# Optimization experiments

Measured on AMD Instinct MI355X. Metric: run time of the kernel, lower is better.

The kernel has to match this reference:

```python
import jax, jax.numpy as jnp
import numpy as np

COST_CLASS = 1.0
COST_COORD = 1.0
ALPHA = 0.25
GAMMA = 2.0
EPS = 1e-8
B, N = 4, 512


def setup_inputs() -> dict:
    key = jax.random.key(0)
    k1, k2, k3 = jax.random.split(key, 3)
    return {
        "pred_logits": jax.random.normal(k1, (B, N), dtype=jnp.float32),
        "pred_points": jax.random.uniform(k2, (B, N, 2), dtype=jnp.float32),
        "gt_points": jax.random.uniform(k3, (B, N, 2), dtype=jnp.float32),
        "gt_mask": jnp.ones((B, N), dtype=bool),
    }


def _cost_matrix(pred_logits, pred_points, gt_points):
    # focal-style classification cost, depends only on the prediction -> column-constant
    prob = jax.nn.sigmoid(pred_logits)                       # [B, N]
    neg = (1.0 - ALPHA) * prob ** GAMMA * (-jnp.log(1.0 - prob + EPS))
    pos = ALPHA * (1.0 - prob) ** GAMMA * (-jnp.log(prob + EPS))
    cost_class = (pos - neg)[:, :, None]                     # [B, N, 1]
    # L1 cdist between pred_points and gt_points
    cost_coord = jnp.sum(
        jnp.abs(pred_points[:, :, None, :] - gt_points[:, None, :, :]), axis=-1
    )                                                        # [B, N, N]
    return COST_CLASS * cost_class + COST_COORD * cost_coord


def _lsa(cost):
    # Jonker-Volgenant shortest augmenting path (e-maxx Hungarian), square, minimization.
    c = np.asarray(cost, dtype=np.float64)
    n = c.shape[0]
    INF = 1e18
    u = np.zeros(n + 1)
    v = np.zeros(n + 1)
    p = np.zeros(n + 1, dtype=np.int64)   # p[j] = row matched to column j (1-based)
    way = np.zeros(n + 1, dtype=np.int64)
    for i in range(1, n + 1):
        p[0] = i
        j0 = 0
        minv = np.full(n + 1, INF)
        used = np.zeros(n + 1, dtype=bool)
        while True:
            used[j0] = True
            i0 = p[j0]
            cur = c[i0 - 1] - u[i0] - v[1:]
            nu = ~used[1:]
            mv = minv[1:]
            wy = way[1:]
            upd = nu & (cur < mv)
            mv[upd] = cur[upd]
            wy[upd] = j0
            cand = np.where(nu, mv, INF)
            j1 = int(np.argmin(cand)) + 1
            delta = cand[j1 - 1]
            u[p[used]] += delta
            v[used] -= delta
            mv[nu] -= delta
            j0 = j1
            if p[j0] == 0:
                break
        while j0:
            j1 = int(way[j0])
            p[j0] = int(p[j1])
            j0 = j1
    col_of_row = np.empty(n, dtype=np.int64)
    col_of_row[p[1:] - 1] = np.arange(n)
    return np.arange(n), col_of_row


def reference(pred_logits, pred_points, gt_points, gt_mask):
    C = _cost_matrix(pred_logits, pred_points, gt_points)   # [B, N, N]
    mask = np.asarray(gt_mask)
    assert mask.all(), "reference assumes all gt slots valid (static shapes)"
    Cn = np.asarray(jax.device_get(C))
    pred_idx, gt_idx = [], []
    for b in range(Cn.shape[0]):
        r, c = _lsa(Cn[b])
        pred_idx.append(r)
        gt_idx.append(c)
    pred_idx = jnp.asarray(np.stack(pred_idx))
    gt_idx = jnp.asarray(np.stack(gt_idx))
    return pred_idx, gt_idx, C
```

## Files before the change

kernel.cpp:

```cpp
#include <hip/hip_runtime.h>
#include <math.h>

constexpr int B_ = 4;
constexpr int N_ = 512;

__device__ __forceinline__ float cephes_expf(float xin) {
#pragma clang fp contract(off)
    float x = fminf(xin, 88.3762626647950f);
    x = fmaxf(x, -88.3762626647949f);
    float fx = x * 1.44269504088896341f;
    fx = fx + 0.5f;
    fx = floorf(fx);
    float tmp = fx * 0.693359375f;
    float z0  = fx * -2.12194440e-4f;
    float r = x - tmp;
    r = r - z0;
    float zz = r * r;
    float y = 1.9875691500E-4f;
    y = y * r + 1.3981999507E-3f;
    y = y * r + 8.3334519073E-3f;
    y = y * r + 4.1665795894E-2f;
    y = y * r + 1.6666665459E-1f;
    y = y * r + 5.0000001201E-1f;
    y = y * zz + r;
    y = y + 1.0f;
    int n = (int)fx;
    float p2n = __uint_as_float((unsigned)(n + 0x7f) << 23);
    float res = y * p2n;
    return fmaxf(res, xin);
}

__device__ __forceinline__ float cephes_logf(float t) {
#pragma clang fp contract(off)
    float xx = fmaxf(t, 1.17549435e-38f);
    unsigned u = __float_as_uint(xx);
    int e_i = (int)(u >> 23) - 0x7f;
    float e = (float)e_i + 1.0f;
    float m = __uint_as_float((u & 0x807fffffu) | 0x3f000000u);
    int mask = (m < 0.707106781186547524f);
    float tmp1 = mask ? m : 0.0f;
    float x = m - 1.0f;
    e = e - (mask ? 1.0f : 0.0f);
    x = x + tmp1;
    float z = x * x;
    float y = 7.0376836292E-2f;
    y = y * x + -1.1514610310E-1f;
    y = y * x + 1.1676998740E-1f;
    y = y * x + -1.2420140846E-1f;
    y = y * x + 1.4249322787E-1f;
    y = y * x + -1.6668057665E-1f;
    y = y * x + 2.0000714765E-1f;
    y = y * x + -2.4999993993E-1f;
    y = y * x + 3.3333331174E-1f;
    y = y * x;
    y = y * z;
    y = e * -2.12194440e-4f + y;
    y = y - z * 0.5f;
    float res = x + y;
    res = res + e * 0.693359375f;
    return res;
}

__global__ __launch_bounds__(256) void class_cost_kernel(
    const float* __restrict__ logits, float* __restrict__ cc_out)
{
#pragma clang fp contract(off)
    int idx = blockIdx.x * 256 + threadIdx.x;
    if (idx >= B_ * N_) return;
    float x    = logits[idx];
    float e    = cephes_expf(-x);
    float prob = 1.0f / (1.0f + e);
    float om   = 1.0f - prob;
    float p2   = prob * prob;
    float o2   = om * om;
    float lneg = cephes_logf(om   + 1e-8f);
    float lpos = cephes_logf(prob + 1e-8f);
    float neg  = (0.75f * p2) * (-lneg);
    float pos  = (0.25f * o2) * (-lpos);
    cc_out[idx] = pos - neg;
}

__global__ __launch_bounds__(512) void cost_kernel(
    const float* __restrict__ cc,
    const float* __restrict__ pred_pts,
    const float* __restrict__ gt_pts,
    float* __restrict__ C)
{
    int blk = blockIdx.x;
    int b = blk >> 9;
    int i = blk & (N_ - 1);
    int j = threadIdx.x;

    const float2* pp2 = reinterpret_cast<const float2*>(pred_pts);
    const float2* gp2 = reinterpret_cast<const float2*>(gt_pts);
    float2 pp = pp2[b * N_ + i];
    float2 gp = gp2[b * N_ + j];
    float coord = fabsf(pp.x - gp.x) + fabsf(pp.y - gp.y);

    C[(size_t)b * N_ * N_ + (size_t)i * N_ + j] = cc[blk] + coord;
}

template<int CTRL>
__device__ __forceinline__ uint32_t dpp32(uint32_t x) {
    return (uint32_t)__builtin_amdgcn_update_dpp((int)x, (int)x, CTRL, 0xF, 0xF, false);
}
#define UMINSTEP(X, CTRL) { uint32_t o_ = dpp32<CTRL>(X); X = (o_ < X) ? o_ : X; }

__device__ __forceinline__ uint32_t wave_umin_lane63(uint32_t x) {
    UMINSTEP(x, 0x111) UMINSTEP(x, 0x112) UMINSTEP(x, 0x114)
    UMINSTEP(x, 0x118) UMINSTEP(x, 0x142) UMINSTEP(x, 0x143)
    return x;
}

__device__ __forceinline__ double readlane_f64(double d, int lane) {
    unsigned long long ll = (unsigned long long)__double_as_longlong(d);
    unsigned lo = (unsigned)__builtin_amdgcn_readlane((int)(unsigned)ll, lane);
    unsigned hi = (unsigned)__builtin_amdgcn_readlane((int)(unsigned)(ll >> 32), lane);
    return __longlong_as_double((long long)(((unsigned long long)hi << 32) | lo));
}

__global__ __launch_bounds__(64) void solve_kernel(
    const float* __restrict__ cc_in,
    const float* __restrict__ pred_pts,
    const float* __restrict__ gt_pts,
    float* __restrict__ pred_idx,
    float* __restrict__ gt_idx)
{
    const int b = blockIdx.x;
    const int t = threadIdx.x;

    const float2* pq = reinterpret_cast<const float2*>(pred_pts) + b * N_;
    const float2* gq = reinterpret_cast<const float2*>(gt_pts)   + b * N_;
    const float*  cq = cc_in + b * N_;
    const int base = t << 3;

    float2 r0 = pq[base + 0], r1 = pq[base + 1], r2 = pq[base + 2], r3 = pq[base + 3];
    float2 r4 = pq[base + 4], r5 = pq[base + 5], r6 = pq[base + 6], r7 = pq[base + 7];
    float2 g0 = gq[base + 0], g1 = gq[base + 1], g2 = gq[base + 2], g3 = gq[base + 3];
    float2 g4 = gq[base + 4], g5 = gq[base + 5], g6 = gq[base + 6], g7 = gq[base + 7];
    float  c0 = cq[base + 0], c1 = cq[base + 1], c2 = cq[base + 2], c3 = cq[base + 3];
    float  c4 = cq[base + 4], c5 = cq[base + 5], c6 = cq[base + 6], c7 = cq[base + 7];

    double u0=0.0,u1=0.0,u2=0.0,u3=0.0,u4=0.0,u5=0.0,u6=0.0,u7=0.0;
    double v0=0.0,v1=0.0,v2=0.0,v3=0.0,v4=0.0,v5=0.0,v6=0.0,v7=0.0;
    int    p0=-1,p1=-1,p2=-1,p3=-1,p4=-1,p5=-1,p6=-1,p7=-1;

    #pragma unroll
    for (int k = 0; k < 8; ++k)
        pred_idx[b * N_ + t + 64 * k] = (float)(t + 64 * k);

    #define SEL8F(sl, x0,x1,x2,x3,x4,x5,x6,x7, out) {                      \
        float a0_=((sl)&1)?(x1):(x0), a1_=((sl)&1)?(x3):(x2);              \
        float a2_=((sl)&1)?(x5):(x4), a3_=((sl)&1)?(x7):(x6);              \
        float b0_=((sl)&2)?a1_:a0_,   b1_=((sl)&2)?a3_:a2_;                \
        out = ((sl)&4)?b1_:b0_; }
    #define SEL8I(sl, x0,x1,x2,x3,x4,x5,x6,x7, out) {                      \
        int a0_=((sl)&1)?(x1):(x0), a1_=((sl)&1)?(x3):(x2);                \
        int a2_=((sl)&1)?(x5):(x4), a3_=((sl)&1)?(x7):(x6);                \
        int b0_=((sl)&2)?a1_:a0_,   b1_=((sl)&2)?a3_:a2_;                  \
        out = ((sl)&4)?b1_:b0_; }
    #define SEL8D(sl, x0,x1,x2,x3,x4,x5,x6,x7, out) {                      \
        double a0_=((sl)&1)?(x1):(x0), a1_=((sl)&1)?(x3):(x2);             \
        double a2_=((sl)&1)?(x5):(x4), a3_=((sl)&1)?(x7):(x6);             \
        double b0_=((sl)&2)?a1_:a0_,   b1_=((sl)&2)?a3_:a2_;               \
        out = ((sl)&4)?b1_:b0_; }

    float px_r, py_r, cc_r; double urow;
    #define ROW_SCALARS(r) {                                               \
        int sl_ = (r) & 7, ln_ = (r) >> 3;                                 \
        float sx_, sy_, sc_; double su_;                                   \
        SEL8F(sl_, r0.x,r1.x,r2.x,r3.x,r4.x,r5.x,r6.x,r7.x, sx_);          \
        SEL8F(sl_, r0.y,r1.y,r2.y,r3.y,r4.y,r5.y,r6.y,r7.y, sy_);          \
        SEL8F(sl_, c0,c1,c2,c3,c4,c5,c6,c7, sc_);                          \
        SEL8D(sl_, u0,u1,u2,u3,u4,u5,u6,u7, su_);                          \
        px_r = __uint_as_float((unsigned)__builtin_amdgcn_readlane(        \
                   (int)__float_as_uint(sx_), ln_));                       \
        py_r = __uint_as_float((unsigned)__builtin_amdgcn_readlane(        \
                   (int)__float_as_uint(sy_), ln_));                       \
        cc_r = __uint_as_float((unsigned)__builtin_amdgcn_readlane(        \
                   (int)__float_as_uint(sc_), ln_));                       \
        urow = readlane_f64(su_, ln_); }

    const float INF32 = __uint_as_float(0x7F800000u);

    for (int i = 0; i < N_; ++i) {
        unsigned used_m  = 0u;
        unsigned chain_m = (t == (i >> 3)) ? (1u << (i & 7)) : 0u;
        ROW_SCALARS(i);

        for (;;) {
#pragma clang fp contract(off)
            float w0 = cc_r + (fabsf(px_r - g0.x) + fabsf(py_r - g0.y));
            float w1 = cc_r + (fabsf(px_r - g1.x) + fabsf(py_r - g1.y));
            float w2 = cc_r + (fabsf(px_r - g2.x) + fabsf(py_r - g2.y));
            float w3 = cc_r + (fabsf(px_r - g3.x) + fabsf(py_r - g3.y));
            float w4 = cc_r + (fabsf(px_r - g4.x) + fabsf(py_r - g4.y));
            float w5 = cc_r + (fabsf(px_r - g5.x) + fabsf(py_r - g5.y));
            float w6 = cc_r + (fabsf(px_r - g6.x) + fabsf(py_r - g6.y));
            float w7 = cc_r + (fabsf(px_r - g7.x) + fabsf(py_r - g7.y));
            w0 = (used_m & 0x01u) ? INF32 : w0;
            w1 = (used_m & 0x02u) ? INF32 : w1;
            w2 = (used_m & 0x04u) ? INF32 : w2;
            w3 = (used_m & 0x08u) ? INF32 : w3;
            w4 = (used_m & 0x10u) ? INF32 : w4;
            w5 = (used_m & 0x20u) ? INF32 : w5;
            w6 = (used_m & 0x40u) ? INF32 : w6;
            w7 = (used_m & 0x80u) ? INF32 : w7;

            double d0 = ((double)w0 - urow) - v0;
            double d1 = ((double)w1 - urow) - v1;
            double d2 = ((double)w2 - urow) - v2;
            double d3 = ((double)w3 - urow) - v3;
            double d4 = ((double)w4 - urow) - v4;
            double d5 = ((double)w5 - urow) - v5;
            double d6 = ((double)w6 - urow) - v6;
            double d7 = ((double)w7 - urow) - v7;

            double  ka = (d1 < d0) ? d1 : d0;  uint32_t sa = (d1 < d0) ? 1u : 0u;
            double  kb = (d3 < d2) ? d3 : d2;  uint32_t sb = (d3 < d2) ? 3u : 2u;
            double  kx = (d5 < d4) ? d5 : d4;  uint32_t sx = (d5 < d4) ? 5u : 4u;
            double  kd = (d7 < d6) ? d7 : d6;  uint32_t sd = (d7 < d6) ? 7u : 6u;
            double  ke = (kb < ka) ? kb : ka;  uint32_t se = (kb < ka) ? sb : sa;
            double  kf = (kd < kx) ? kd : kx;  uint32_t sf = (kd < kx) ? sd : sx;
            double  bv = (kf < ke) ? kf : ke;  uint32_t bslot = (kf < ke) ? sf : se;

            uint64_t kb64 = (uint64_t)__double_as_longlong(bv);
            kb64 ^= (kb64 >> 63) ? 0xFFFFFFFFFFFFFFFFull : 0x8000000000000000ull;
            uint32_t khi = (uint32_t)(kb64 >> 32);
            uint32_t klo = (uint32_t)kb64;

            int own_pre;
            SEL8I(bslot, p0,p1,p2,p3,p4,p5,p6,p7, own_pre);

            uint32_t Mhi = (uint32_t)__builtin_amdgcn_readlane(
                               (int)wave_umin_lane63(khi), 63);
            unsigned long long tied_hi = __ballot(khi == Mhi);

            int lane1; uint32_t Mlo;
            if (__builtin_popcountll(tied_hi) == 1) {
                lane1 = (int)__builtin_ctzll(tied_hi);
                Mlo = (uint32_t)__builtin_amdgcn_readlane((int)klo, lane1);
            } else {
                uint32_t kl2 = (khi == Mhi) ? klo : 0xFFFFFFFFu;
                Mlo = (uint32_t)__builtin_amdgcn_readlane(
                          (int)wave_umin_lane63(kl2), 63);
                lane1 = (int)__builtin_ctzll(__ballot(khi == Mhi && klo == Mlo));
            }

            int slot1 = __builtin_amdgcn_readlane((int)bslot, lane1);
            int owner = __builtin_amdgcn_readlane(own_pre, lane1);

            uint64_t M = ((uint64_t)Mhi << 32) | Mlo;
            uint64_t db = (M >> 63) ? (M ^ 0x8000000000000000ull) : ~M;
            double delta = __longlong_as_double((long long)db);

            if (owner < 0) {
                u0 += (chain_m & 0x01u) ? delta : 0.0;
                u1 += (chain_m & 0x02u) ? delta : 0.0;
                u2 += (chain_m & 0x04u) ? delta : 0.0;
                u3 += (chain_m & 0x08u) ? delta : 0.0;
                u4 += (chain_m & 0x10u) ? delta : 0.0;
                u5 += (chain_m & 0x20u) ? delta : 0.0;
                u6 += (chain_m & 0x40u) ? delta : 0.0;
                u7 += (chain_m & 0x80u) ? delta : 0.0;
                v0 -= (used_m  & 0x01u) ? delta : 0.0;
                v1 -= (used_m  & 0x02u) ? delta : 0.0;
                v2 -= (used_m  & 0x04u) ? delta : 0.0;
                v3 -= (used_m  & 0x08u) ? delta : 0.0;
                v4 -= (used_m  & 0x10u) ? delta : 0.0;
                v5 -= (used_m  & 0x20u) ? delta : 0.0;
                v6 -= (used_m  & 0x40u) ? delta : 0.0;
                v7 -= (used_m  & 0x80u) ? delta : 0.0;
                bool mine = (t == lane1);
                p0 = (mine && slot1 == 0) ? i : p0;
                p1 = (mine && slot1 == 1) ? i : p1;
                p2 = (mine && slot1 == 2) ? i : p2;
                p3 = (mine && slot1 == 3) ? i : p3;
                p4 = (mine && slot1 == 4) ? i : p4;
                p5 = (mine && slot1 == 5) ? i : p5;
                p6 = (mine && slot1 == 6) ? i : p6;
                p7 = (mine && slot1 == 7) ? i : p7;
                break;
            }

            ROW_SCALARS(owner);

            u0 += (chain_m & 0x01u) ? delta : 0.0;
            u1 += (chain_m & 0x02u) ? delta : 0.0;
            u2 += (chain_m & 0x04u) ? delta : 0.0;
            u3 += (chain_m & 0x08u) ? delta : 0.0;
            u4 += (chain_m & 0x10u) ? delta : 0.0;
            u5 += (chain_m & 0x20u) ? delta : 0.0;
            u6 += (chain_m & 0x40u) ? delta : 0.0;
            u7 += (chain_m & 0x80u) ? delta : 0.0;
            v0 -= (used_m  & 0x01u) ? delta : 0.0;
            v1 -= (used_m  & 0x02u) ? delta : 0.0;
            v2 -= (used_m  & 0x04u) ? delta : 0.0;
            v3 -= (used_m  & 0x08u) ? delta : 0.0;
            v4 -= (used_m  & 0x10u) ? delta : 0.0;
            v5 -= (used_m  & 0x20u) ? delta : 0.0;
            v6 -= (used_m  & 0x40u) ? delta : 0.0;
            v7 -= (used_m  & 0x80u) ? delta : 0.0;

            used_m  |= (t == lane1)        ? (1u << slot1)       : 0u;
            chain_m |= (t == (owner >> 3)) ? (1u << (owner & 7)) : 0u;
        }
    }

    gt_idx[b * N_ + p0] = (float)(base);
    gt_idx[b * N_ + p1] = (float)(base + 1);
    gt_idx[b * N_ + p2] = (float)(base + 2);
    gt_idx[b * N_ + p3] = (float)(base + 3);
    gt_idx[b * N_ + p4] = (float)(base + 4);
    gt_idx[b * N_ + p5] = (float)(base + 5);
    gt_idx[b * N_ + p6] = (float)(base + 6);
    gt_idx[b * N_ + p7] = (float)(base + 7);
}

extern "C" void kernel_launch(void* const* d_in, const int* in_sizes, int n_in,
                              void* d_out, int out_size, void* d_ws, size_t ws_size,
                              hipStream_t stream)
{
    const float* logits   = (const float*)d_in[0];
    const float* pred_pts = (const float*)d_in[1];
    const float* gt_pts   = (const float*)d_in[2];

    float* out      = (float*)d_out;
    float* pred_idx = out;
    float* gt_idx   = out + B_ * N_;
    float* C        = out + 2 * B_ * N_;
    float* cc       = (float*)d_ws;

    class_cost_kernel<<<(B_ * N_ + 255) / 256, 256, 0, stream>>>(logits, cc);
    cost_kernel<<<B_ * N_, N_, 0, stream>>>(cc, pred_pts, gt_pts, C);
    solve_kernel<<<B_, 64, 0, stream>>>(cc, pred_pts, gt_pts, pred_idx, gt_idx);
}
```

Baseline: 1.645 ms.

## Run all batch solves in one block, co-locating waves on one SIMD

Launches the assignment solver as a single 1024-thread block and reads the hardware wave ID to find which SIMD each wave runs on. The four batch solves are assigned to waves that share the most populated SIMD; all other waves exit. This concentrates the serial solves on one CU/SIMD, possibly for shared cache locality, at the risk of the waves contending for one SIMD's issue bandwidth.

```diff
diff --git a/kernel.cpp b/kernel.cpp
--- a/kernel.cpp
+++ b/kernel.cpp
@@ -119,15 +119,46 @@
     return __longlong_as_double((long long)(((unsigned long long)hi << 32) | lo));
 }
 
-__global__ __launch_bounds__(64) void solve_kernel(
+#define HWID_GETREG_IMM (4 | (0 << 6) | (31 << 11))
+
+__global__ __launch_bounds__(1024) void solve_kernel(
     const float* __restrict__ cc_in,
     const float* __restrict__ pred_pts,
     const float* __restrict__ gt_pts,
     float* __restrict__ pred_idx,
     float* __restrict__ gt_idx)
 {
-    const int b = blockIdx.x;
-    const int t = threadIdx.x;
+    const int wave = threadIdx.x >> 6;
+    const int t    = threadIdx.x & 63;
+
+    unsigned hwid = (unsigned)__builtin_amdgcn_s_getreg(HWID_GETREG_IMM);
+    int my_simd = (int)((hwid >> 4) & 3u);
+
+    __shared__ int simd_of[16];
+    if (t == 0) simd_of[wave] = my_simd;
+    __syncthreads();
+
+    int cnt0 = 0, cnt1 = 0, cnt2 = 0, cnt3 = 0;
+    #pragma unroll
+    for (int w = 0; w < 16; ++w) {
+        int s = simd_of[w];
+        cnt0 += (s == 0); cnt1 += (s == 1); cnt2 += (s == 2); cnt3 += (s == 3);
+    }
+    int best = 0, bestc = cnt0;
+    if (cnt1 > bestc) { best = 1; bestc = cnt1; }
+    if (cnt2 > bestc) { best = 2; bestc = cnt2; }
+    if (cnt3 > bestc) { best = 3; bestc = cnt3; }
+
+    int b = -1, rank = 0;
+    #pragma unroll
+    for (int w = 0; w < 16; ++w) {
+        if (simd_of[w] == best) {
+            if (w == wave && rank < 4) b = rank;
+            ++rank;
+        }
+    }
+    if (b < 0) return;
+
 
     const float2* pq = reinterpret_cast<const float2*>(pred_pts) + b * N_;
     const float2* gq = reinterpret_cast<const float2*>(gt_pts)   + b * N_;
@@ -333,5 +364,5 @@
 
     class_cost_kernel<<<(B_ * N_ + 255) / 256, 256, 0, stream>>>(logits, cc);
     cost_kernel<<<B_ * N_, N_, 0, stream>>>(cc, pred_pts, gt_pts, C);
-    solve_kernel<<<B_, 64, 0, stream>>>(cc, pred_pts, gt_pts, pred_idx, gt_idx);
-}
+    solve_kernel<<<1, 1024, 0, stream>>>(cc, pred_pts, gt_pts, pred_idx, gt_idx);
+}
```

Measured after the change: 4.505 ms. 174% more time.
